# Kernel optimization log

Hardware: AMD Instinct MI355X
Metric: run time of the kernel (lower is better)

Reference implementation:

```python
import jax, jax.numpy as jnp
import numpy as np

B, T, D, H = 2, 2048, 768, 12
HD = D // H  # head_dim = 64


def setup_inputs() -> dict:
    key = jax.random.key(0)
    ks = jax.random.split(key, 5)
    s = 0.02
    return {
        "x": jax.random.normal(ks[0], (B, T, D), dtype=jnp.float32),
        "w_qkv": jax.random.normal(ks[1], (D, 3 * D), dtype=jnp.float32) * s,
        "b_qkv": jax.random.normal(ks[2], (3 * D,), dtype=jnp.float32) * s,
        "w_out": jax.random.normal(ks[3], (D, D), dtype=jnp.float32) * s,
        "b_out": jax.random.normal(ks[4], (D,), dtype=jnp.float32) * s,
    }


def reference(x, w_qkv, b_qkv, w_out, b_out):
    Bx, Tx, C = x.shape
    qkv = x @ w_qkv + b_qkv                       # [B,T,3C]
    q, k, v = jnp.split(qkv, 3, axis=-1)
    # [B,H,T,hd]
    q = q.reshape(Bx, Tx, H, HD).transpose(0, 2, 1, 3)
    k = k.reshape(Bx, Tx, H, HD).transpose(0, 2, 1, 3)
    v = v.reshape(Bx, Tx, H, HD).transpose(0, 2, 1, 3)
    scale = 1.0 / jnp.sqrt(jnp.float32(HD))
    attn = jnp.einsum('bhqd,bhkd->bhqk', q, k) * scale  # [B,H,T,T]
    causal = jnp.tril(jnp.ones((Tx, Tx), dtype=bool))
    attn = jnp.where(causal, attn, -jnp.inf)
    attn = jax.nn.softmax(attn, axis=-1)
    y = jnp.einsum('bhqk,bhkd->bhqd', attn, v)          # [B,H,T,hd]
    y = y.transpose(0, 2, 1, 3).reshape(Bx, Tx, C)
    return y @ w_out + b_out
```

## Files before the change

kernel.cpp:

```cpp
#include <hip/hip_runtime.h>
#include <math.h>

typedef __attribute__((ext_vector_type(8))) __bf16 bf16x8;
typedef __attribute__((ext_vector_type(4))) __bf16 bf16x4;
typedef __attribute__((ext_vector_type(4))) float f32x4;

#define GLOAD_LDS16(gsrc, ldst) \
  __builtin_amdgcn_global_load_lds((__attribute__((address_space(1))) const void*)(gsrc), \
                                   (__attribute__((address_space(3))) void*)(ldst), 16, 0, 0)

__device__ __forceinline__ float fexp2(float x) {
#if __has_builtin(__builtin_amdgcn_exp2f)
  return __builtin_amdgcn_exp2f(x);
#else
  return exp2f(x);
#endif
}

__global__ void cvt_bf16_kernel(const float* __restrict__ in, __bf16* __restrict__ out, int n4) {
  int i = blockIdx.x * 256 + threadIdx.x;
  if (i < n4) {
    float4 f = ((const float4*)in)[i];
    bf16x4 o;
    o[0] = (__bf16)f.x; o[1] = (__bf16)f.y; o[2] = (__bf16)f.z; o[3] = (__bf16)f.w;
    ((bf16x4*)out)[i] = o;
  }
}

__global__ __launch_bounds__(256)
void cvtT_bf16_kernel(const float* __restrict__ in, __bf16* __restrict__ out, int R, int C) {
  __shared__ float t[32][33];
  int c0 = blockIdx.x * 32, r0 = blockIdx.y * 32;
  int tc = threadIdx.x & 31, tr = threadIdx.x >> 5;
#pragma unroll
  for (int i = 0; i < 4; ++i)
    t[tr + 8 * i][tc] = in[(size_t)(r0 + tr + 8 * i) * C + c0 + tc];
  __syncthreads();
#pragma unroll
  for (int i = 0; i < 4; ++i)
    out[(size_t)(c0 + tr + 8 * i) * R + r0 + tc] = (__bf16)t[tc][tr + 8 * i];
}

template<int EPI, int BM, int BN, int WAVES, int WGM, int WGN, int BUFS>
__global__ __launch_bounds__(WAVES * 64, 3)
void gemm_tn_kernel(const __bf16* __restrict__ A, const __bf16* __restrict__ Bm,
                    const float* __restrict__ bias, float* __restrict__ outF,
                    __bf16* __restrict__ qo, __bf16* __restrict__ ko, __bf16* __restrict__ vo,
                    int M, int N, int K, int NBX, int NNX, int PPX) {
  constexpr int NTA = BM / 16, NTB = BN / 16;
  constexpr int NA = 2 * NTA;
  constexpr int NSEG = 2 * NTA + 2 * NTB;
  constexpr int LPTH = (NSEG + WAVES - 1) / WAVES;
  constexpr int LPTR = NSEG % WAVES;
  constexpr int LLO = (LPTR == 0) ? LPTH : LPTH - 1;
  constexpr int AM = NTA / WGM;
  constexpr int BNF = NTB / WGN;
  const int lane = threadIdx.x & 63;
  const int wave = threadIdx.x >> 6;
  const int r16 = lane & 15, g = lane >> 4;
  const int id = blockIdx.x;
  const int xcd = id & 7, slot = id >> 3;
  const int nxn = NBX / NNX;
  const int mg = xcd / nxn, ng = xcd % nxn;
  const int lp = slot / NNX, ln = slot - (slot / NNX) * NNX;
  const int mBase = (mg * PPX + lp) * BM, nBase = (ng * NNX + ln) * BN;
  __shared__ __align__(16) __bf16 lds[BUFS][NSEG * 512];

  f32x4 acc[AM][BNF];
#pragma unroll
  for (int i = 0; i < AM; ++i)
#pragma unroll
    for (int j = 0; j < BNF; ++j) acc[i][j] = (f32x4){0.f, 0.f, 0.f, 0.f};

  const int mw = (wave / WGN) * AM;
  const int nw = (wave % WGN) * BNF;

  auto stage = [&](int ke, int b) {
#pragma unroll
    for (int i = 0; i < LPTH; ++i) {
      int s = wave + i * WAVES;
      if (LPTR == 0 || s < NSEG) {
        int isB = (s >= NA);
        int sb = isB ? s - NA : s;
        int nt = isB ? NTB : NTA;
        int ks = sb / nt, t8 = sb - ks * nt;
        int row = (isB ? nBase : mBase) + t8 * 16 + r16;
        const __bf16* src = (isB ? Bm : A) + (size_t)row * K + ke + ks * 32 + g * 8;
        GLOAD_LDS16(src, &lds[b][s * 512]);
      }
    }
  };

  auto mfma_step = [&](const __bf16* L) {
#pragma unroll
    for (int ks = 0; ks < 2; ++ks) {
      bf16x8 af[AM], bfr[BNF];
#pragma unroll
      for (int i = 0; i < AM; ++i)
        af[i] = *(const bf16x8*)&L[((ks * NTA + mw + i) * 64 + lane) * 8];
#pragma unroll
      for (int j = 0; j < BNF; ++j)
        bfr[j] = *(const bf16x8*)&L[((NA + ks * NTB + nw + j) * 64 + lane) * 8];
      __builtin_amdgcn_s_setprio(1);
#pragma unroll
      for (int i = 0; i < AM; ++i)
#pragma unroll
        for (int j = 0; j < BNF; ++j)
          acc[i][j] = __builtin_amdgcn_mfma_f32_16x16x32_bf16(af[i], bfr[j], acc[i][j], 0, 0, 0);
      __builtin_amdgcn_s_setprio(0);
    }
  };

  const int nt = K >> 6;
  if constexpr (BUFS == 2) {
    stage(0, 0);
    int cur = 0;
    for (int t = 0; t < nt; ++t) {
      __syncthreads();
      if (t + 1 < nt) stage((t + 1) << 6, cur ^ 1);
      mfma_step(lds[cur]);
      cur ^= 1;
    }
  } else {
    stage(0, 0);
    stage(64, 1);
    int cur = 0;
    for (int t = 0; t < nt; ++t) {
      if (t + 1 < nt) {
        if (LPTR != 0 && wave < LPTR) asm volatile("s_waitcnt vmcnt(%0)" :: "i"(LPTH) : "memory");
        else                          asm volatile("s_waitcnt vmcnt(%0)" :: "i"(LLO) : "memory");
      } else {
        asm volatile("s_waitcnt vmcnt(0)" ::: "memory");
      }
      __builtin_amdgcn_sched_barrier(0);
      __builtin_amdgcn_s_barrier();
      __builtin_amdgcn_sched_barrier(0);
      int nxt = cur + 2; if (nxt >= 3) nxt -= 3;
      if (t + 2 < nt) stage((t + 2) << 6, nxt);
      mfma_step(lds[cur]);
      if (++cur == 3) cur = 0;
    }
  }

#pragma unroll
  for (int i = 0; i < AM; ++i) {
#pragma unroll
    for (int j = 0; j < BNF; ++j) {
      int c = nBase + (nw + j) * 16 + r16;
      float bb = bias[c];
#pragma unroll
      for (int e = 0; e < 4; ++e) {
        int r = mBase + (mw + i) * 16 + g * 4 + e;
        float val = acc[i][j][e] + bb;
        if (EPI == 0) {
          int which = c / 768;
          int cc = c - which * 768;
          int hh = cc >> 6, dd = cc & 63;
          int bI = r >> 11, tt = r & 2047;
          if (which == 0) {
            qo[(((size_t)(bI * 12 + hh)) * 2048 + tt) * 64 + dd] = (__bf16)(val * 0.180336880f);
          } else if (which == 1) {
            ko[(((size_t)(bI * 12 + hh)) * 2048 + tt) * 64 + dd] = (__bf16)val;
          } else {
            vo[(((size_t)(bI * 12 + hh)) * 64 + dd) * 2048 + tt] = (__bf16)val;
          }
        } else {
          outF[(size_t)r * N + c] = val;
        }
      }
    }
  }
}

__global__ __launch_bounds__(256, 2)
void attn_kernel(const __bf16* __restrict__ qg, const __bf16* __restrict__ kg,
                 const __bf16* __restrict__ vtg, __bf16* __restrict__ yatt) {
  const int id = blockIdx.x;
  const int chunk = id & 7, within = id >> 3;
  const int bh = chunk * 3 + (within >> 5);
  const int a = within & 31, p = 63 - a;
  const int Ka = (a >> 1) + 1, Kp = (p >> 1) + 1;
  const int lane = threadIdx.x & 63, wave = threadIdx.x >> 6;
  const int r16 = lane & 15, g = lane >> 4;
  const int bI = bh / 12, h = bh - bI * 12;
  const size_t headoff = (size_t)bh * 2048 * 64;
  const __bf16* Q = qg + headoff;
  const __bf16* Kh = kg + headoff;
  const __bf16* VT = vtg + headoff;

  __shared__ __align__(16) __bf16 Kbuf[2][4096];
  __shared__ __align__(16) __bf16 Vbuf[2][4096];
  __shared__ __align__(16) __bf16 Plds[4][16][72];

  const int myTile = (wave < 2) ? p : a;
  const int myKt   = (wave < 2) ? Kp : Ka;
  const int rowQ   = myTile * 32 + (wave & 1) * 16 + r16;

  bf16x8 qf[2];
#pragma unroll
  for (int ks = 0; ks < 2; ++ks)
    qf[ks] = *(const bf16x8*)&Q[(size_t)rowQ * 64 + ks * 32 + g * 8];

  int srow[2], scl[2];
#pragma unroll
  for (int i = 0; i < 2; ++i) {
    int c = (i * 4 + wave) * 64 + lane;
    srow[i] = c >> 3;
    scl[i] = (c & 7) ^ (srow[i] & 7);
  }
  auto stage = [&](int kt, int b) {
#pragma unroll
    for (int i = 0; i < 2; ++i) {
      GLOAD_LDS16(&Kh[(size_t)(kt * 64 + srow[i]) * 64 + scl[i] * 8], &Kbuf[b][(i * 4 + wave) * 512]);
      GLOAD_LDS16(&VT[(size_t)srow[i] * 2048 + kt * 64 + scl[i] * 8], &Vbuf[b][(i * 4 + wave) * 512]);
    }
  };

  f32x4 o[4];
#pragma unroll
  for (int j = 0; j < 4; ++j) o[j] = (f32x4){0.f, 0.f, 0.f, 0.f};
  float l = 0.f;

  stage(0, 0);
  for (int kt = 0; kt < Kp; ++kt) {
    const int cur = kt & 1;
    __syncthreads();
    if (kt + 1 < Kp) stage(kt + 1, cur ^ 1);
    if (kt < myKt) {
      f32x4 st[4];
#pragma unroll
      for (int j = 0; j < 4; ++j) st[j] = (f32x4){0.f, 0.f, 0.f, 0.f};
      __builtin_amdgcn_s_setprio(1);
#pragma unroll
      for (int ks = 0; ks < 2; ++ks)
#pragma unroll
        for (int j = 0; j < 4; ++j) {
          int row = j * 16 + r16;
          int cp = (ks * 4 + g) ^ (row & 7);
          bf16x8 kf = *(const bf16x8*)&Kbuf[cur][(row * 8 + cp) * 8];
          st[j] = __builtin_amdgcn_mfma_f32_16x16x32_bf16(kf, qf[ks], st[j], 0, 0, 0);
        }
      __builtin_amdgcn_s_setprio(0);
      bf16x8 vf[2][4];
#pragma unroll
      for (int ks = 0; ks < 2; ++ks)
#pragma unroll
        for (int dj = 0; dj < 4; ++dj) {
          int row = dj * 16 + r16;
          int cp = (ks * 4 + g) ^ (row & 7);
          vf[ks][dj] = *(const bf16x8*)&Vbuf[cur][(row * 8 + cp) * 8];
        }
      if (kt == myKt - 1) {
#pragma unroll
        for (int j = 0; j < 4; ++j)
#pragma unroll
          for (int e = 0; e < 4; ++e)
            if (kt * 64 + j * 16 + 4 * g + e > rowQ) st[j][e] = -INFINITY;
      }
      float ls = 0.f;
#pragma unroll
      for (int j = 0; j < 4; ++j)
#pragma unroll
        for (int e = 0; e < 4; ++e) {
          float pv = fexp2(st[j][e]);
          st[j][e] = pv;
          ls += pv;
        }
      ls += __shfl_xor(ls, 16, 64);
      ls += __shfl_xor(ls, 32, 64);
      l += ls;
#pragma unroll
      for (int j = 0; j < 4; ++j) {
        bf16x4 pk;
#pragma unroll
        for (int e = 0; e < 4; ++e) pk[e] = (__bf16)st[j][e];
        *(bf16x4*)&Plds[wave][r16][j * 16 + 4 * g] = pk;
      }
      __builtin_amdgcn_s_setprio(1);
#pragma unroll
      for (int ks = 0; ks < 2; ++ks) {
        bf16x8 pf = *(const bf16x8*)&Plds[wave][r16][ks * 32 + g * 8];
#pragma unroll
        for (int dj = 0; dj < 4; ++dj)
          o[dj] = __builtin_amdgcn_mfma_f32_16x16x32_bf16(vf[ks][dj], pf, o[dj], 0, 0, 0);
      }
      __builtin_amdgcn_s_setprio(0);
    }
  }

  float inv = 1.0f / l;
#pragma unroll
  for (int dj = 0; dj < 4; ++dj) {
    bf16x4 ov;
#pragma unroll
    for (int e = 0; e < 4; ++e) ov[e] = (__bf16)(o[dj][e] * inv);
    *(bf16x4*)&yatt[((size_t)(bI * 2048 + rowQ)) * 768 + h * 64 + dj * 16 + 4 * g] = ov;
  }
}

extern "C" void kernel_launch(void* const* d_in, const int* in_sizes, int n_in,
                              void* d_out, int out_size, void* d_ws, size_t ws_size,
                              hipStream_t stream) {
  (void)in_sizes; (void)n_in; (void)out_size; (void)ws_size;
  const float* x     = (const float*)d_in[0];
  const float* w_qkv = (const float*)d_in[1];
  const float* b_qkv = (const float*)d_in[2];
  const float* w_out = (const float*)d_in[3];
  const float* b_out = (const float*)d_in[4];
  float* out = (float*)d_out;

  char* ws = (char*)d_ws;
  __bf16* xb    = (__bf16*)(ws);
  __bf16* wqkvT = (__bf16*)(ws + 6291456);
  __bf16* woT   = (__bf16*)(ws + 9830400);
  __bf16* qb    = (__bf16*)(ws + 11010048);
  __bf16* kb    = (__bf16*)(ws + 17301504);
  __bf16* vtb   = (__bf16*)(ws + 23592960);
  __bf16* yatt  = (__bf16*)(ws + 29884416);

  cvt_bf16_kernel<<<3072, 256, 0, stream>>>(x, xb, 786432);
  cvtT_bf16_kernel<<<dim3(72, 24), 256, 0, stream>>>(w_qkv, wqkvT, 768, 2304);
  cvtT_bf16_kernel<<<dim3(24, 24), 256, 0, stream>>>(w_out, woT, 768, 768);
  gemm_tn_kernel<0, 128, 144, 6, 2, 3, 2><<<512, 384, 0, stream>>>(
      xb, wqkvT, b_qkv, nullptr, qb, kb, vtb, 4096, 2304, 768, 16, 2, 32);
  attn_kernel<<<768, 256, 0, stream>>>(qb, kb, vtb, yatt);
  gemm_tn_kernel<1, 64, 96, 4, 2, 2, 3><<<512, 256, 0, stream>>>(
      yatt, woT, b_out, out, nullptr, nullptr, nullptr, 4096, 768, 768, 8, 4, 16);
}
```

Before: 118.0 us.

## Process two 16-row Q sub-tiles per wave in attention and widen QKV GEMM tiles

Each attention wave now owns a full 32-row query tile and computes two 16-row sub-tiles against each staged K/V block. This reuses the K fragments and V loads across twice the rows and halves the attention grid to 384 blocks, each pairing four tiles so causal work stays balanced. The QKV projection GEMM switches to larger 128x288 tiles with 768 threads and 256 blocks. The cost is more registers per wave and fewer blocks to fill the GPU, which the raised launch-bounds occupancy hint may not offset.

```diff
diff --git a/kernel.cpp b/kernel.cpp
--- a/kernel.cpp
+++ b/kernel.cpp
@@ -172,14 +172,13 @@
   }
 }
 
-__global__ __launch_bounds__(256, 2)
+__global__ __launch_bounds__(256, 3)
 void attn_kernel(const __bf16* __restrict__ qg, const __bf16* __restrict__ kg,
                  const __bf16* __restrict__ vtg, __bf16* __restrict__ yatt) {
   const int id = blockIdx.x;
   const int chunk = id & 7, within = id >> 3;
-  const int bh = chunk * 3 + (within >> 5);
-  const int a = within & 31, p = 63 - a;
-  const int Ka = (a >> 1) + 1, Kp = (p >> 1) + 1;
+  const int bh = chunk * 3 + (within >> 4);
+  const int u = within & 15;
   const int lane = threadIdx.x & 63, wave = threadIdx.x >> 6;
   const int r16 = lane & 15, g = lane >> 4;
   const int bI = bh / 12, h = bh - bI * 12;
@@ -192,14 +191,20 @@
   __shared__ __align__(16) __bf16 Vbuf[2][4096];
   __shared__ __align__(16) __bf16 Plds[4][16][72];
 
-  const int myTile = (wave < 2) ? p : a;
-  const int myKt   = (wave < 2) ? Kp : Ka;
-  const int rowQ   = myTile * 32 + (wave & 1) * 16 + r16;
-
-  bf16x8 qf[2];
-#pragma unroll
-  for (int ks = 0; ks < 2; ++ks)
-    qf[ks] = *(const bf16x8*)&Q[(size_t)rowQ * 64 + ks * 32 + g * 8];
+  const int myTile = (wave == 0) ? (63 - 2 * u) : (wave == 1) ? (62 - 2 * u)
+                   : (wave == 2) ? (2 * u)      : (2 * u + 1);
+  const int myKt = (myTile >> 1) + 1;
+  const int Kmax = 32 - u;
+
+  const int row0 = myTile * 32 + r16;
+  const int row1 = myTile * 32 + 16 + r16;
+
+  bf16x8 qf[2][2];
+#pragma unroll
+  for (int ks = 0; ks < 2; ++ks) {
+    qf[0][ks] = *(const bf16x8*)&Q[(size_t)row0 * 64 + ks * 32 + g * 8];
+    qf[1][ks] = *(const bf16x8*)&Q[(size_t)row1 * 64 + ks * 32 + g * 8];
+  }
 
   int srow[2], scl[2];
 #pragma unroll
@@ -216,20 +221,20 @@
     }
   };
 
-  f32x4 o[4];
-#pragma unroll
-  for (int j = 0; j < 4; ++j) o[j] = (f32x4){0.f, 0.f, 0.f, 0.f};
-  float l = 0.f;
+  f32x4 o0[4], o1[4];
+#pragma unroll
+  for (int j = 0; j < 4; ++j) { o0[j] = (f32x4){0.f,0.f,0.f,0.f}; o1[j] = (f32x4){0.f,0.f,0.f,0.f}; }
+  float l0 = 0.f, l1 = 0.f;
 
   stage(0, 0);
-  for (int kt = 0; kt < Kp; ++kt) {
+  for (int kt = 0; kt < Kmax; ++kt) {
     const int cur = kt & 1;
     __syncthreads();
-    if (kt + 1 < Kp) stage(kt + 1, cur ^ 1);
+    if (kt + 1 < Kmax) stage(kt + 1, cur ^ 1);
     if (kt < myKt) {
-      f32x4 st[4];
-#pragma unroll
-      for (int j = 0; j < 4; ++j) st[j] = (f32x4){0.f, 0.f, 0.f, 0.f};
+      f32x4 st0[4], st1[4];
+#pragma unroll
+      for (int j = 0; j < 4; ++j) { st0[j] = (f32x4){0.f,0.f,0.f,0.f}; st1[j] = (f32x4){0.f,0.f,0.f,0.f}; }
       __builtin_amdgcn_s_setprio(1);
 #pragma unroll
       for (int ks = 0; ks < 2; ++ks)
@@ -238,7 +243,8 @@
           int row = j * 16 + r16;
           int cp = (ks * 4 + g) ^ (row & 7);
           bf16x8 kf = *(const bf16x8*)&Kbuf[cur][(row * 8 + cp) * 8];
-          st[j] = __builtin_amdgcn_mfma_f32_16x16x32_bf16(kf, qf[ks], st[j], 0, 0, 0);
+          st0[j] = __builtin_amdgcn_mfma_f32_16x16x32_bf16(kf, qf[0][ks], st0[j], 0, 0, 0);
+          st1[j] = __builtin_amdgcn_mfma_f32_16x16x32_bf16(kf, qf[1][ks], st1[j], 0, 0, 0);
         }
       __builtin_amdgcn_s_setprio(0);
       bf16x8 vf[2][4];
@@ -250,30 +256,34 @@
           int cp = (ks * 4 + g) ^ (row & 7);
           vf[ks][dj] = *(const bf16x8*)&Vbuf[cur][(row * 8 + cp) * 8];
         }
-      if (kt == myKt - 1) {
+      const bool lastT = (kt == myKt - 1);
+      if (lastT) {
 #pragma unroll
         for (int j = 0; j < 4; ++j)
 #pragma unroll
-          for (int e = 0; e < 4; ++e)
-            if (kt * 64 + j * 16 + 4 * g + e > rowQ) st[j][e] = -INFINITY;
-      }
-      float ls = 0.f;
+          for (int e = 0; e < 4; ++e) {
+            int k = kt * 64 + j * 16 + 4 * g + e;
+            if (k > row0) st0[j][e] = -INFINITY;
+            if (k > row1) st1[j][e] = -INFINITY;
+          }
+      }
+      float ls0 = 0.f, ls1 = 0.f;
 #pragma unroll
       for (int j = 0; j < 4; ++j)
 #pragma unroll
         for (int e = 0; e < 4; ++e) {
-          float pv = fexp2(st[j][e]);
-          st[j][e] = pv;
-          ls += pv;
+          float p0 = fexp2(st0[j][e]);
+          float p1 = fexp2(st1[j][e]);
+          st0[j][e] = p0; ls0 += p0;
+          st1[j][e] = p1; ls1 += p1;
         }
-      ls += __shfl_xor(ls, 16, 64);
-      ls += __shfl_xor(ls, 32, 64);
-      l += ls;
+      ls0 += __shfl_xor(ls0, 16, 64); ls0 += __shfl_xor(ls0, 32, 64); l0 += ls0;
+      ls1 += __shfl_xor(ls1, 16, 64); ls1 += __shfl_xor(ls1, 32, 64); l1 += ls1;
 #pragma unroll
       for (int j = 0; j < 4; ++j) {
         bf16x4 pk;
 #pragma unroll
-        for (int e = 0; e < 4; ++e) pk[e] = (__bf16)st[j][e];
+        for (int e = 0; e < 4; ++e) pk[e] = (__bf16)st0[j][e];
         *(bf16x4*)&Plds[wave][r16][j * 16 + 4 * g] = pk;
       }
       __builtin_amdgcn_s_setprio(1);
@@ -282,19 +292,36 @@
         bf16x8 pf = *(const bf16x8*)&Plds[wave][r16][ks * 32 + g * 8];
 #pragma unroll
         for (int dj = 0; dj < 4; ++dj)
-          o[dj] = __builtin_amdgcn_mfma_f32_16x16x32_bf16(vf[ks][dj], pf, o[dj], 0, 0, 0);
+          o0[dj] = __builtin_amdgcn_mfma_f32_16x16x32_bf16(vf[ks][dj], pf, o0[dj], 0, 0, 0);
       }
       __builtin_amdgcn_s_setprio(0);
-    }
-  }
-
-  float inv = 1.0f / l;
+#pragma unroll
+      for (int j = 0; j < 4; ++j) {
+        bf16x4 pk;
+#pragma unroll
+        for (int e = 0; e < 4; ++e) pk[e] = (__bf16)st1[j][e];
+        *(bf16x4*)&Plds[wave][r16][j * 16 + 4 * g] = pk;
+      }
+      __builtin_amdgcn_s_setprio(1);
+#pragma unroll
+      for (int ks = 0; ks < 2; ++ks) {
+        bf16x8 pf = *(const bf16x8*)&Plds[wave][r16][ks * 32 + g * 8];
+#pragma unroll
+        for (int dj = 0; dj < 4; ++dj)
+          o1[dj] = __builtin_amdgcn_mfma_f32_16x16x32_bf16(vf[ks][dj], pf, o1[dj], 0, 0, 0);
+      }
+      __builtin_amdgcn_s_setprio(0);
+    }
+  }
+
+  float inv0 = 1.0f / l0, inv1 = 1.0f / l1;
 #pragma unroll
   for (int dj = 0; dj < 4; ++dj) {
-    bf16x4 ov;
-#pragma unroll
-    for (int e = 0; e < 4; ++e) ov[e] = (__bf16)(o[dj][e] * inv);
-    *(bf16x4*)&yatt[((size_t)(bI * 2048 + rowQ)) * 768 + h * 64 + dj * 16 + 4 * g] = ov;
+    bf16x4 ov0, ov1;
+#pragma unroll
+    for (int e = 0; e < 4; ++e) { ov0[e] = (__bf16)(o0[dj][e] * inv0); ov1[e] = (__bf16)(o1[dj][e] * inv1); }
+    *(bf16x4*)&yatt[((size_t)(bI * 2048 + row0)) * 768 + h * 64 + dj * 16 + 4 * g] = ov0;
+    *(bf16x4*)&yatt[((size_t)(bI * 2048 + row1)) * 768 + h * 64 + dj * 16 + 4 * g] = ov1;
   }
 }
 
@@ -321,9 +348,9 @@
   cvt_bf16_kernel<<<3072, 256, 0, stream>>>(x, xb, 786432);
   cvtT_bf16_kernel<<<dim3(72, 24), 256, 0, stream>>>(w_qkv, wqkvT, 768, 2304);
   cvtT_bf16_kernel<<<dim3(24, 24), 256, 0, stream>>>(w_out, woT, 768, 768);
-  gemm_tn_kernel<0, 128, 144, 6, 2, 3, 2><<<512, 384, 0, stream>>>(
-      xb, wqkvT, b_qkv, nullptr, qb, kb, vtb, 4096, 2304, 768, 16, 2, 32);
-  attn_kernel<<<768, 256, 0, stream>>>(qb, kb, vtb, yatt);
+  gemm_tn_kernel<0, 128, 288, 12, 2, 6, 3><<<256, 768, 0, stream>>>(
+      xb, wqkvT, b_qkv, nullptr, qb, kb, vtb, 4096, 2304, 768, 8, 1, 32);
+  attn_kernel<<<384, 256, 0, stream>>>(qb, kb, vtb, yatt);
   gemm_tn_kernel<1, 64, 96, 4, 2, 2, 3><<<512, 256, 0, stream>>>(
       yatt, woT, b_out, out, nullptr, nullptr, nullptr, 4096, 768, 768, 8, 4, 16);
 }
```

New measurement: 116.7 us. No clear change (-1.2%).
